# Kernel optimization log

Hardware: AMD Instinct MI355X
Metric: run time of the kernel (lower is better)

Reference implementation:

```python
import jax, jax.numpy as jnp
import numpy as np

NUM_NODES = 20000
EMB_DIM = 128
HIDDEN = 64
NUM_RELS = 8
NUM_CLASSES = 16
HEADS = 3
NUM_EDGES = 640000
NEG_SLOPE = 0.2


def setup_inputs() -> dict:
    key = jax.random.key(0)
    ks = jax.random.split(key, 12)
    edge_index = jax.random.randint(ks[0], (2, NUM_EDGES), 0, NUM_NODES, dtype=jnp.int32)
    edge_type = jax.random.randint(ks[1], (NUM_EDGES,), 0, NUM_RELS, dtype=jnp.int32)
    s1 = 1.0 / np.sqrt(EMB_DIM)
    s2 = 1.0 / np.sqrt(HIDDEN)
    return {
        "emb": jax.random.normal(ks[2], (NUM_NODES, EMB_DIM), jnp.float32),
        "w1": jax.random.normal(ks[3], (NUM_RELS, EMB_DIM, HEADS * HIDDEN), jnp.float32) * s1,
        "q1": jax.random.normal(ks[4], (HEADS * HIDDEN, HEADS), jnp.float32) * s2,
        "k1": jax.random.normal(ks[5], (HEADS * HIDDEN, HEADS), jnp.float32) * s2,
        "b1": jnp.zeros((HIDDEN,), jnp.float32),
        "w2": jax.random.normal(ks[6], (NUM_RELS, HIDDEN, HEADS * NUM_CLASSES), jnp.float32) * s2,
        "q2": jax.random.normal(ks[7], (HEADS * NUM_CLASSES, HEADS), jnp.float32) * 0.1,
        "k2": jax.random.normal(ks[8], (HEADS * NUM_CLASSES, HEADS), jnp.float32) * 0.1,
        "b2": jnp.zeros((NUM_CLASSES,), jnp.float32),
        "edge_index": edge_index,
        "edge_type": edge_type,
    }


def _rgat_conv(x, w, q, k, b, src, dst, edge_type, heads, out_ch):
    # Per-relation node transform [R, N, heads*out]; equivalent to x_e @ w[edge_type[e]]
    n = x.shape[0]
    xr = jnp.einsum('nd,rdo->rno', x, w)
    out_i = xr[edge_type, dst]  # [E, heads*out] (destination, x_i)
    out_j = xr[edge_type, src]  # [E, heads*out] (source, x_j)
    # additive self-attention with dim=1: alpha [E, heads]
    alpha = jax.nn.leaky_relu(out_i @ q + out_j @ k, negative_slope=NEG_SLOPE)
    # across-relation segment softmax over destination index (PyG utils.softmax)
    amax = jax.ops.segment_max(alpha, dst, num_segments=n)
    amax = jnp.where(jnp.isneginf(amax), 0.0, amax)
    ex = jnp.exp(alpha - amax[dst])
    denom = jax.ops.segment_sum(ex, dst, num_segments=n)
    alpha = ex / (denom[dst] + 1e-16)
    # weighted messages, scatter-add aggregation
    msg = alpha[:, :, None] * out_j.reshape(-1, heads, out_ch)  # [E, heads, out]
    aggr = jax.ops.segment_sum(msg, dst, num_segments=n)  # [N, heads, out]
    # concat=False -> mean over heads, then bias [out]
    return aggr.mean(axis=1) + b


def reference(emb, w1, q1, k1, b1, w2, q2, k2, b2, edge_index, edge_type):
    src, dst = edge_index[0], edge_index[1]
    x1 = _rgat_conv(emb, w1, q1, k1, b1, src, dst, edge_type, HEADS, HIDDEN)
    x2 = jax.nn.relu(x1)
    x3 = _rgat_conv(x2, w2, q2, k2, b2, src, dst, edge_type, HEADS, NUM_CLASSES)
    return jax.nn.sigmoid(x3)
```

## Files before the change

kernel.cpp:

```cpp
#include <hip/hip_runtime.h>
#include <hip/hip_bf16.h>
#include <math.h>

#define N_NODES 20000
#define EMB 128
#define HID 64
#define RELS 8
#define CLS 16
#define N_EDGES 640000
#define NEG 0.2f
#define NKEYS (N_NODES * RELS)
#define SCAN_CHUNK 1024
#define SCAN_NBLK ((NKEYS + SCAN_CHUNK - 1) / SCAN_CHUNK)

typedef unsigned short ushort_t;
typedef __attribute__((ext_vector_type(8))) short bf16x8;
typedef __attribute__((ext_vector_type(8))) unsigned short ushort8_t;
typedef __attribute__((ext_vector_type(4))) unsigned short ushort4_t;
typedef __attribute__((ext_vector_type(4))) float f32x4;

__device__ __forceinline__ float b2f(ushort_t u) {
    return __uint_as_float(((unsigned int)u) << 16);
}
__device__ __forceinline__ ushort_t f2b(float f) {
    __hip_bfloat16 h = __float2bfloat16(f);
    return *reinterpret_cast<ushort_t*>(&h);
}

__global__ __launch_bounds__(256) void k_cvt(const float* __restrict__ in, ushort_t* __restrict__ outp, int n4) {
    int i = blockIdx.x * blockDim.x + threadIdx.x;
    if (i >= n4) return;
    float4 v = *(const float4*)&in[(size_t)i * 4];
    ushort4 o;
    o.x = f2b(v.x); o.y = f2b(v.y); o.z = f2b(v.z); o.w = f2b(v.w);
    *(ushort4*)&outp[(size_t)i * 4] = o;
}

template <int D, int OUT>
__global__ __launch_bounds__(256) void k_wqk(const float* __restrict__ w, const float* __restrict__ q,
                                             const float* __restrict__ k, ushort_t* __restrict__ wqkt) {
    int tid = blockIdx.x * blockDim.x + threadIdx.x;
    if (tid >= 48 * D) return;
    int c = tid / D, i = tid % D;
    int r = c / 6, j = c % 6;
    const float* qk = (j < 3) ? q : k;
    int jj = (j < 3) ? j : j - 3;
    const float* wrow = w + ((size_t)r * D + i) * OUT;
    float s = 0.f;
    for (int o = 0; o < OUT; o++) s += wrow[o] * qk[o * 3 + jj];
    wqkt[(size_t)c * D + i] = f2b(s);
}

template <int D, int OC>
__global__ __launch_bounds__(256) void k_wagg(const float* __restrict__ w, ushort_t* __restrict__ outp) {
    const int KT = RELS * 3 * D;
    int tid = blockIdx.x * blockDim.x + threadIdx.x;
    if (tid >= OC * KT) return;
    int o = tid / KT, kidx = tid % KT;
    int r = kidx / (3 * D), h = (kidx / D) % 3, i = kidx % D;
    float v = w[((size_t)r * D + i) * (3 * OC) + h * OC + o];
    outp[tid] = f2b(v);
}

__global__ __launch_bounds__(256) void k_count(const int* __restrict__ dst, const int* __restrict__ et,
                                               int* __restrict__ counts) {
    int e = blockIdx.x * blockDim.x + threadIdx.x;
    if (e < N_EDGES) atomicAdd(&counts[dst[e] * 8 + et[e]], 1);
}

__global__ __launch_bounds__(256) void k_scanA(const int* __restrict__ counts, int* __restrict__ keyoff,
                                               int* __restrict__ blocksum) {
    __shared__ int part[256];
    int b = blockIdx.x, tid = threadIdx.x;
    int base = b * SCAN_CHUNK + tid * 4;
    int4 c = make_int4(0, 0, 0, 0);
    if (base + 3 < NKEYS) c = *(const int4*)&counts[base];
    else {
        if (base + 0 < NKEYS) c.x = counts[base + 0];
        if (base + 1 < NKEYS) c.y = counts[base + 1];
        if (base + 2 < NKEYS) c.z = counts[base + 2];
        if (base + 3 < NKEYS) c.w = counts[base + 3];
    }
    int s = c.x + c.y + c.z + c.w;
    part[tid] = s;
    __syncthreads();
    for (int off = 1; off < 256; off <<= 1) {
        int v = (tid >= off) ? part[tid - off] : 0;
        __syncthreads();
        part[tid] += v;
        __syncthreads();
    }
    int excl = part[tid] - s;
    int4 o;
    o.x = excl;
    o.y = excl + c.x;
    o.z = excl + c.x + c.y;
    o.w = excl + c.x + c.y + c.z;
    if (base + 3 < NKEYS) *(int4*)&keyoff[base] = o;
    else {
        if (base + 0 < NKEYS) keyoff[base + 0] = o.x;
        if (base + 1 < NKEYS) keyoff[base + 1] = o.y;
        if (base + 2 < NKEYS) keyoff[base + 2] = o.z;
        if (base + 3 < NKEYS) keyoff[base + 3] = o.w;
    }
    if (tid == 255) blocksum[b] = part[255];
}

__global__ __launch_bounds__(256) void k_scanB(int* __restrict__ blocksum, int* __restrict__ blockbase,
                                               int* __restrict__ keyoff) {
    __shared__ int part[256];
    int tid = threadIdx.x;
    int v0 = (tid < SCAN_NBLK) ? blocksum[tid] : 0;
    part[tid] = v0;
    __syncthreads();
    for (int off = 1; off < 256; off <<= 1) {
        int v = (tid >= off) ? part[tid - off] : 0;
        __syncthreads();
        part[tid] += v;
        __syncthreads();
    }
    if (tid < SCAN_NBLK) blockbase[tid] = part[tid] - v0;
    if (tid == 255) keyoff[NKEYS] = part[255];
}

__global__ __launch_bounds__(256) void k_scanC(const int* __restrict__ blockbase, int* __restrict__ keyoff,
                                               int* __restrict__ cursor) {
    int b = blockIdx.x, tid = threadIdx.x;
    int base = b * SCAN_CHUNK + tid * 4;
    int add = blockbase[b];
    if (base + 3 < NKEYS) {
        int4 v = *(const int4*)&keyoff[base];
        v.x += add; v.y += add; v.z += add; v.w += add;
        *(int4*)&keyoff[base] = v;
        *(int4*)&cursor[base] = v;
    } else {
        for (int j = 0; j < 4; j++) {
            if (base + j < NKEYS) {
                int v = keyoff[base + j] + add;
                keyoff[base + j] = v;
                cursor[base + j] = v;
            }
        }
    }
}

__global__ __launch_bounds__(256) void k_scatter(const int* __restrict__ src, const int* __restrict__ dst,
                                                 const int* __restrict__ et, int* __restrict__ cursor,
                                                 int* __restrict__ srcs) {
    int e = blockIdx.x * blockDim.x + threadIdx.x;
    if (e < N_EDGES) {
        int p = atomicAdd(&cursor[dst[e] * 8 + et[e]], 1);
        srcs[p] = src[e];
    }
}

template <int K, int KCH, int N, int MREP, int NREP>
__global__ __launch_bounds__(256) void k_mfma_gemm(const ushort_t* __restrict__ A, const ushort_t* __restrict__ Bt,
                                                   float* __restrict__ outp, int M) {
    const int wid = threadIdx.x >> 6;
    const int lane = threadIdx.x & 63;
    const int m0 = blockIdx.x * (4 * MREP * 16) + wid * (MREP * 16);
    const int kbase = blockIdx.y * KCH;
    const int l15 = lane & 15;
    const int kq = (lane >> 4) * 8;

    f32x4 acc[MREP][NREP] = {};
    for (int kk = kbase; kk < kbase + KCH; kk += 32) {
        bf16x8 a[MREP], b[NREP];
#pragma unroll
        for (int i = 0; i < MREP; i++) {
            int row = m0 + i * 16 + l15;
            row = row < M ? row : M - 1;
            a[i] = *(const bf16x8*)&A[(size_t)row * K + kk + kq];
        }
#pragma unroll
        for (int j = 0; j < NREP; j++) b[j] = *(const bf16x8*)&Bt[(size_t)(j * 16 + l15) * K + kk + kq];
#pragma unroll
        for (int i = 0; i < MREP; i++)
#pragma unroll
            for (int j = 0; j < NREP; j++)
                acc[i][j] = __builtin_amdgcn_mfma_f32_16x16x32_bf16(a[i], b[j], acc[i][j], 0, 0, 0);
    }
    float* op = outp + (size_t)blockIdx.y * M * N;
    const int r4 = (lane >> 4) * 4;
#pragma unroll
    for (int i = 0; i < MREP; i++) {
#pragma unroll
        for (int j = 0; j < NREP; j++) {
#pragma unroll
            for (int g = 0; g < 4; g++) {
                int row = m0 + i * 16 + r4 + g;
                if (row < M) op[(size_t)row * N + j * 16 + l15] = acc[i][j][g];
            }
        }
    }
}

__device__ __forceinline__ void edge_alpha(int s_idx, const int (&ko)[9], const int* __restrict__ srcs,
                                           const float* __restrict__ qkd, const float* __restrict__ qbase,
                                           float& a0, float& a1, float& a2, int& sv) {
    int r = 0;
#pragma unroll
    for (int j = 1; j < 8; j++) r += (s_idx >= ko[j]) ? 1 : 0;
    sv = srcs[s_idx];
    const float* kd = qkd + (size_t)sv * 48 + r * 6 + 3;
    const float* qd = qbase + r * 6;
    float t0 = qd[0] + kd[0], t1 = qd[1] + kd[1], t2 = qd[2] + kd[2];
    a0 = t0 > 0.f ? t0 : NEG * t0;
    a1 = t1 > 0.f ? t1 : NEG * t1;
    a2 = t2 > 0.f ? t2 : NEG * t2;
}

__global__ __launch_bounds__(256) void k_stats(const int* __restrict__ keyoff, const int* __restrict__ srcs,
                                               const float* __restrict__ qkd, float4* __restrict__ svw) {
    int node = blockIdx.x * 4 + (threadIdx.x >> 6);
    int lane = threadIdx.x & 63;
    int ko[9];
#pragma unroll
    for (int j = 0; j < 9; j++) ko[j] = keyoff[node * 8 + j];
    int beg = ko[0], end = ko[8], deg = end - beg;
    if (deg == 0) return;
    const float* qbase = qkd + (size_t)node * 48;

    if (deg <= 64) {
        float a0 = -INFINITY, a1 = -INFINITY, a2 = -INFINITY;
        int sv = 0;
        if (lane < deg) edge_alpha(beg + lane, ko, srcs, qkd, qbase, a0, a1, a2, sv);
        float m0 = a0, m1 = a1, m2 = a2;
#pragma unroll
        for (int off = 32; off >= 1; off >>= 1) {
            m0 = fmaxf(m0, __shfl_xor(m0, off));
            m1 = fmaxf(m1, __shfl_xor(m1, off));
            m2 = fmaxf(m2, __shfl_xor(m2, off));
        }
        float e0 = 0.f, e1 = 0.f, e2 = 0.f;
        if (lane < deg) {
            e0 = expf(a0 - m0);
            e1 = expf(a1 - m1);
            e2 = expf(a2 - m2);
        }
        float s0 = e0, s1 = e1, s2 = e2;
#pragma unroll
        for (int off = 32; off >= 1; off >>= 1) {
            s0 += __shfl_xor(s0, off);
            s1 += __shfl_xor(s1, off);
            s2 += __shfl_xor(s2, off);
        }
        float i0 = 1.f / (3.f * (s0 + 1e-16f));
        float i1 = 1.f / (3.f * (s1 + 1e-16f));
        float i2 = 1.f / (3.f * (s2 + 1e-16f));
        if (lane < deg)
            svw[beg + lane] = make_float4(__int_as_float(sv), e0 * i0, e1 * i1, e2 * i2);
    } else {
        float m0 = -INFINITY, m1 = -INFINITY, m2 = -INFINITY;
        for (int i = beg + lane; i < end; i += 64) {
            float a0, a1, a2; int sv;
            edge_alpha(i, ko, srcs, qkd, qbase, a0, a1, a2, sv);
            m0 = fmaxf(m0, a0); m1 = fmaxf(m1, a1); m2 = fmaxf(m2, a2);
        }
#pragma unroll
        for (int off = 32; off >= 1; off >>= 1) {
            m0 = fmaxf(m0, __shfl_xor(m0, off));
            m1 = fmaxf(m1, __shfl_xor(m1, off));
            m2 = fmaxf(m2, __shfl_xor(m2, off));
        }
        float s0 = 0.f, s1 = 0.f, s2 = 0.f;
        for (int i = beg + lane; i < end; i += 64) {
            float a0, a1, a2; int sv;
            edge_alpha(i, ko, srcs, qkd, qbase, a0, a1, a2, sv);
            s0 += expf(a0 - m0); s1 += expf(a1 - m1); s2 += expf(a2 - m2);
        }
#pragma unroll
        for (int off = 32; off >= 1; off >>= 1) {
            s0 += __shfl_xor(s0, off);
            s1 += __shfl_xor(s1, off);
            s2 += __shfl_xor(s2, off);
        }
        float i0 = 1.f / (3.f * (s0 + 1e-16f));
        float i1 = 1.f / (3.f * (s1 + 1e-16f));
        float i2 = 1.f / (3.f * (s2 + 1e-16f));
        for (int i = beg + lane; i < end; i += 64) {
            float a0, a1, a2; int sv;
            edge_alpha(i, ko, srcs, qkd, qbase, a0, a1, a2, sv);
            svw[i] = make_float4(__int_as_float(sv), expf(a0 - m0) * i0, expf(a1 - m1) * i1, expf(a2 - m2) * i2);
        }
    }
}

#define PADK1 408
__global__ __launch_bounds__(256) void k_fused1(const int* __restrict__ keyoff, const float4* __restrict__ svw,
                                                const ushort_t* __restrict__ x, const ushort_t* __restrict__ wagg,
                                                float* __restrict__ part) {
    __shared__ ushort_t lt[16][PADK1];
    const int tid = threadIdx.x;
    const int w = tid >> 6, lane = tid & 63;
    const int q15 = lane & 15, kq = (lane >> 4) * 8;
    const int l15 = lane & 15;
    const int nbase = blockIdx.x * 16;
    const int r = blockIdx.y;
    const int mynode = w * 4 + (lane >> 4);
    const int key = (nbase + mynode) * 8 + r;

    const int beg = keyoff[key], end = keyoff[key + 1];
    float a0[8] = {}, a1[8] = {}, a2[8] = {};
    for (int s = beg; s < end; s++) {
        float4 sw = svw[s];
        int sv = __float_as_int(sw.x);
        ushort8_t xv = *(const ushort8_t*)&x[(size_t)sv * 128 + q15 * 8];
#pragma unroll
        for (int c = 0; c < 8; c++) {
            float f = b2f(xv[c]);
            a0[c] += sw.y * f;
            a1[c] += sw.z * f;
            a2[c] += sw.w * f;
        }
    }
    ushort8_t o0, o1, o2;
#pragma unroll
    for (int c = 0; c < 8; c++) {
        o0[c] = f2b(a0[c]);
        o1[c] = f2b(a1[c]);
        o2[c] = f2b(a2[c]);
    }
    *(ushort8_t*)&lt[mynode][0 * 128 + q15 * 8] = o0;
    *(ushort8_t*)&lt[mynode][1 * 128 + q15 * 8] = o1;
    *(ushort8_t*)&lt[mynode][2 * 128 + q15 * 8] = o2;
    __syncthreads();

    f32x4 acc = {};
#pragma unroll
    for (int ks = 0; ks < 12; ks++) {
        bf16x8 av = *(const bf16x8*)&lt[l15][ks * 32 + kq];
        bf16x8 bv = *(const bf16x8*)&wagg[(size_t)(w * 16 + l15) * 3072 + r * 384 + ks * 32 + kq];
        acc = __builtin_amdgcn_mfma_f32_16x16x32_bf16(av, bv, acc, 0, 0, 0);
    }
    float* op = part + (size_t)r * N_NODES * 64;
    const int r4 = (lane >> 4) * 4;
#pragma unroll
    for (int g = 0; g < 4; g++) {
        int row = nbase + r4 + g;
        op[(size_t)row * 64 + w * 16 + l15] = acc[g];
    }
}

#define PADK2 208
__global__ __launch_bounds__(256) void k_fused2(const int* __restrict__ keyoff, const float4* __restrict__ svw,
                                                const ushort_t* __restrict__ x2in, const ushort_t* __restrict__ wagg,
                                                float* __restrict__ part) {
    __shared__ ushort_t lt[16][PADK2];
    const int tid = threadIdx.x;
    const int w = tid >> 6, lane = tid & 63;
    const int q15 = lane & 15, kq = (lane >> 4) * 8;
    const int l15 = lane & 15;
    const int nbase = blockIdx.x * 16;
    const int r = blockIdx.y;
    const int mynode = w * 4 + (lane >> 4);
    const int key = (nbase + mynode) * 8 + r;

    const int beg = keyoff[key], end = keyoff[key + 1];
    float a0[4] = {}, a1[4] = {}, a2[4] = {};
    for (int s = beg; s < end; s++) {
        float4 sw = svw[s];
        int sv = __float_as_int(sw.x);
        ushort4_t xv = *(const ushort4_t*)&x2in[(size_t)sv * 64 + q15 * 4];
#pragma unroll
        for (int c = 0; c < 4; c++) {
            float f = b2f(xv[c]);
            a0[c] += sw.y * f;
            a1[c] += sw.z * f;
            a2[c] += sw.w * f;
        }
    }
    ushort4_t o0, o1, o2;
#pragma unroll
    for (int c = 0; c < 4; c++) {
        o0[c] = f2b(a0[c]);
        o1[c] = f2b(a1[c]);
        o2[c] = f2b(a2[c]);
    }
    *(ushort4_t*)&lt[mynode][0 * 64 + q15 * 4] = o0;
    *(ushort4_t*)&lt[mynode][1 * 64 + q15 * 4] = o1;
    *(ushort4_t*)&lt[mynode][2 * 64 + q15 * 4] = o2;
    __syncthreads();

    if (w == 0) {
        f32x4 acc = {};
#pragma unroll
        for (int ks = 0; ks < 6; ks++) {
            bf16x8 av = *(const bf16x8*)&lt[l15][ks * 32 + kq];
            bf16x8 bv = *(const bf16x8*)&wagg[(size_t)l15 * 1536 + r * 192 + ks * 32 + kq];
            acc = __builtin_amdgcn_mfma_f32_16x16x32_bf16(av, bv, acc, 0, 0, 0);
        }
        const int r4 = (lane >> 4) * 4;
#pragma unroll
        for (int g = 0; g < 4; g++)
            part[(size_t)r * N_NODES * 16 + (size_t)(nbase + r4 + g) * 16 + l15] = acc[g];
    }
}

__global__ __launch_bounds__(256) void k_reduce1(const float* __restrict__ part, const float* __restrict__ bias,
                                                 ushort_t* __restrict__ x2) {
    int idx = blockIdx.x * blockDim.x + threadIdx.x;
    const int MN = N_NODES * 64;
    if (idx >= MN) return;
    float s = bias[idx & 63];
#pragma unroll
    for (int r = 0; r < 8; r++) s += part[idx + (size_t)r * MN];
    x2[idx] = f2b(s > 0.f ? s : 0.f);
}

__global__ __launch_bounds__(256) void k_reduce2(const float* __restrict__ part, const float* __restrict__ bias,
                                                 float* __restrict__ outp) {
    int idx = blockIdx.x * blockDim.x + threadIdx.x;
    const int MN = N_NODES * 16;
    if (idx >= MN) return;
    float s = bias[idx & 15];
#pragma unroll
    for (int r = 0; r < 8; r++) s += part[idx + (size_t)r * MN];
    outp[idx] = 1.f / (1.f + expf(-s));
}

extern "C" void kernel_launch(void* const* d_in, const int* in_sizes, int n_in, void* d_out, int out_size,
                              void* d_ws, size_t ws_size, hipStream_t stream) {
    const float* emb = (const float*)d_in[0];
    const float* w1 = (const float*)d_in[1];
    const float* q1 = (const float*)d_in[2];
    const float* k1 = (const float*)d_in[3];
    const float* b1 = (const float*)d_in[4];
    const float* w2 = (const float*)d_in[5];
    const float* q2 = (const float*)d_in[6];
    const float* k2 = (const float*)d_in[7];
    const float* b2 = (const float*)d_in[8];
    const int* eidx = (const int*)d_in[9];
    const int* etype = (const int*)d_in[10];
    const int* srcv = eidx;
    const int* dstv = eidx + N_EDGES;
    float* out = (float*)d_out;

    char* p = (char*)d_ws;
    auto alloc = [&](size_t bytes) -> void* {
        void* q = p;
        p += (bytes + 255) & ~(size_t)255;
        return q;
    };
    int* counts = (int*)alloc((size_t)NKEYS * 4);
    int* keyoff = (int*)alloc((size_t)(NKEYS + 1) * 4);
    int* cursor = (int*)alloc((size_t)NKEYS * 4);
    int* blocksum = (int*)alloc((size_t)SCAN_NBLK * 4);
    int* blockbase = (int*)alloc((size_t)SCAN_NBLK * 4);
    int* srcs = (int*)alloc((size_t)N_EDGES * 4);
    float4* svw = (float4*)alloc((size_t)N_EDGES * 16);
    ushort_t* emb_b = (ushort_t*)alloc((size_t)N_NODES * EMB * 2);
    ushort_t* wqkt1 = (ushort_t*)alloc((size_t)48 * 128 * 2);
    ushort_t* wagg1 = (ushort_t*)alloc((size_t)64 * 3072 * 2);
    ushort_t* wqkt2 = (ushort_t*)alloc((size_t)48 * 64 * 2);
    ushort_t* wagg2 = (ushort_t*)alloc((size_t)16 * 1536 * 2);
    float* qkd = (float*)alloc((size_t)N_NODES * 48 * 4);
    ushort_t* x2 = (ushort_t*)alloc((size_t)N_NODES * 64 * 2);
    float* partials = (float*)alloc((size_t)8 * N_NODES * 64 * 4);

    k_cvt<<<(N_NODES * EMB / 4 + 255) / 256, 256, 0, stream>>>(emb, emb_b, N_NODES * EMB / 4);
    k_wqk<128, 192><<<(48 * 128 + 255) / 256, 256, 0, stream>>>(w1, q1, k1, wqkt1);
    k_wqk<64, 48><<<(48 * 64 + 255) / 256, 256, 0, stream>>>(w2, q2, k2, wqkt2);
    k_wagg<128, 64><<<(64 * 3072 + 255) / 256, 256, 0, stream>>>(w1, wagg1);
    k_wagg<64, 16><<<(16 * 1536 + 255) / 256, 256, 0, stream>>>(w2, wagg2);

    hipMemsetAsync(counts, 0, (size_t)NKEYS * 4, stream);
    k_count<<<(N_EDGES + 255) / 256, 256, 0, stream>>>(dstv, etype, counts);
    k_scanA<<<SCAN_NBLK, 256, 0, stream>>>(counts, keyoff, blocksum);
    k_scanB<<<1, 256, 0, stream>>>(blocksum, blockbase, keyoff);
    k_scanC<<<SCAN_NBLK, 256, 0, stream>>>(blockbase, keyoff, cursor);
    k_scatter<<<(N_EDGES + 255) / 256, 256, 0, stream>>>(srcv, dstv, etype, cursor, srcs);

    k_mfma_gemm<128, 128, 48, 1, 3><<<dim3(313, 1), 256, 0, stream>>>(emb_b, wqkt1, qkd, N_NODES);
    k_stats<<<N_NODES / 4, 256, 0, stream>>>(keyoff, srcs, qkd, svw);
    k_fused1<<<dim3(N_NODES / 16, 8), 256, 0, stream>>>(keyoff, svw, emb_b, wagg1, partials);
    k_reduce1<<<(N_NODES * 64 + 255) / 256, 256, 0, stream>>>(partials, b1, x2);

    k_mfma_gemm<64, 64, 48, 1, 3><<<dim3(313, 1), 256, 0, stream>>>(x2, wqkt2, qkd, N_NODES);
    k_stats<<<N_NODES / 4, 256, 0, stream>>>(keyoff, srcs, qkd, svw);
    k_fused2<<<dim3(N_NODES / 16, 8), 256, 0, stream>>>(keyoff, svw, x2, wagg2, partials);
    k_reduce2<<<(N_NODES * 16 + 255) / 256, 256, 0, stream>>>(partials, b2, out);
}
```

Before: 262.4 us.

## Merge weight/embedding prep kernels into one launch and software-pipeline gather loops

Result: faster. 243.8 us (-7.1%).

```diff
diff --git a/kernel.cpp b/kernel.cpp
--- a/kernel.cpp
+++ b/kernel.cpp
@@ -27,9 +27,7 @@
     return *reinterpret_cast<ushort_t*>(&h);
 }
 
-__global__ __launch_bounds__(256) void k_cvt(const float* __restrict__ in, ushort_t* __restrict__ outp, int n4) {
-    int i = blockIdx.x * blockDim.x + threadIdx.x;
-    if (i >= n4) return;
+__device__ __forceinline__ void prep_cvt(int i, const float* __restrict__ in, ushort_t* __restrict__ outp) {
     float4 v = *(const float4*)&in[(size_t)i * 4];
     ushort4 o;
     o.x = f2b(v.x); o.y = f2b(v.y); o.z = f2b(v.z); o.w = f2b(v.w);
@@ -37,10 +35,8 @@
 }
 
 template <int D, int OUT>
-__global__ __launch_bounds__(256) void k_wqk(const float* __restrict__ w, const float* __restrict__ q,
-                                             const float* __restrict__ k, ushort_t* __restrict__ wqkt) {
-    int tid = blockIdx.x * blockDim.x + threadIdx.x;
-    if (tid >= 48 * D) return;
+__device__ __forceinline__ void prep_wqk(int tid, const float* __restrict__ w, const float* __restrict__ q,
+                                         const float* __restrict__ k, ushort_t* __restrict__ wqkt) {
     int c = tid / D, i = tid % D;
     int r = c / 6, j = c % 6;
     const float* qk = (j < 3) ? q : k;
@@ -52,14 +48,37 @@
 }
 
 template <int D, int OC>
-__global__ __launch_bounds__(256) void k_wagg(const float* __restrict__ w, ushort_t* __restrict__ outp) {
+__device__ __forceinline__ void prep_wagg(int tid, const float* __restrict__ w, ushort_t* __restrict__ outp) {
     const int KT = RELS * 3 * D;
-    int tid = blockIdx.x * blockDim.x + threadIdx.x;
-    if (tid >= OC * KT) return;
-    int o = tid / KT, kidx = tid % KT;
+    int kidx = tid % KT;
+    int o = tid / KT;
     int r = kidx / (3 * D), h = (kidx / D) % 3, i = kidx % D;
-    float v = w[((size_t)r * D + i) * (3 * OC) + h * OC + o];
-    outp[tid] = f2b(v);
+    outp[tid] = f2b(w[((size_t)r * D + i) * (3 * OC) + h * OC + o]);
+}
+
+#define PREP_N0 (N_NODES * EMB / 4)
+#define PREP_N1 (48 * 128)
+#define PREP_N2 (48 * 64)
+#define PREP_N3 (64 * 3072)
+#define PREP_N4 (16 * 1536)
+#define PREP_TOT (PREP_N0 + PREP_N1 + PREP_N2 + PREP_N3 + PREP_N4)
+
+__global__ __launch_bounds__(256) void k_prep(const float* __restrict__ emb, ushort_t* __restrict__ emb_b,
+                                              const float* __restrict__ w1, const float* __restrict__ q1,
+                                              const float* __restrict__ k1, ushort_t* __restrict__ wqkt1,
+                                              const float* __restrict__ w2, const float* __restrict__ q2,
+                                              const float* __restrict__ k2, ushort_t* __restrict__ wqkt2,
+                                              ushort_t* __restrict__ wagg1, ushort_t* __restrict__ wagg2) {
+    int tid = blockIdx.x * 256 + threadIdx.x;
+    if (tid < PREP_N0) { prep_cvt(tid, emb, emb_b); return; }
+    tid -= PREP_N0;
+    if (tid < PREP_N1) { prep_wqk<128, 192>(tid, w1, q1, k1, wqkt1); return; }
+    tid -= PREP_N1;
+    if (tid < PREP_N2) { prep_wqk<64, 48>(tid, w2, q2, k2, wqkt2); return; }
+    tid -= PREP_N2;
+    if (tid < PREP_N3) { prep_wagg<128, 64>(tid, w1, wagg1); return; }
+    tid -= PREP_N3;
+    if (tid < PREP_N4) { prep_wagg<64, 16>(tid, w2, wagg2); return; }
 }
 
 __global__ __launch_bounds__(256) void k_count(const int* __restrict__ dst, const int* __restrict__ et,
@@ -302,17 +321,35 @@
     const int key = (nbase + mynode) * 8 + r;
 
     const int beg = keyoff[key], end = keyoff[key + 1];
+    const int deg = end - beg;
     float a0[8] = {}, a1[8] = {}, a2[8] = {};
-    for (int s = beg; s < end; s++) {
-        float4 sw = svw[s];
-        int sv = __float_as_int(sw.x);
-        ushort8_t xv = *(const ushort8_t*)&x[(size_t)sv * 128 + q15 * 8];
-#pragma unroll
-        for (int c = 0; c < 8; c++) {
-            float f = b2f(xv[c]);
-            a0[c] += sw.y * f;
-            a1[c] += sw.z * f;
-            a2[c] += sw.w * f;
+    if (deg > 0) {
+        float4 sw0 = svw[beg];
+        float4 sw1;
+        {
+            int s = beg + 1;
+            sw1 = svw[s < end ? s : beg];
+            if (1 >= deg) { sw1.y = 0.f; sw1.z = 0.f; sw1.w = 0.f; }
+        }
+        ushort8_t xv0 = *(const ushort8_t*)&x[(size_t)__float_as_int(sw0.x) * 128 + q15 * 8];
+        for (int i = 0; i < deg; i++) {
+            float4 sw2;
+            {
+                int s = beg + i + 2;
+                sw2 = svw[s < end ? s : beg];
+                if (i + 2 >= deg) { sw2.y = 0.f; sw2.z = 0.f; sw2.w = 0.f; }
+            }
+            ushort8_t xv1 = *(const ushort8_t*)&x[(size_t)__float_as_int(sw1.x) * 128 + q15 * 8];
+#pragma unroll
+            for (int c = 0; c < 8; c++) {
+                float f = b2f(xv0[c]);
+                a0[c] += sw0.y * f;
+                a1[c] += sw0.z * f;
+                a2[c] += sw0.w * f;
+            }
+            sw0 = sw1;
+            sw1 = sw2;
+            xv0 = xv1;
         }
     }
     ushort8_t o0, o1, o2;
@@ -358,17 +395,35 @@
     const int key = (nbase + mynode) * 8 + r;
 
     const int beg = keyoff[key], end = keyoff[key + 1];
+    const int deg = end - beg;
     float a0[4] = {}, a1[4] = {}, a2[4] = {};
-    for (int s = beg; s < end; s++) {
-        float4 sw = svw[s];
-        int sv = __float_as_int(sw.x);
-        ushort4_t xv = *(const ushort4_t*)&x2in[(size_t)sv * 64 + q15 * 4];
-#pragma unroll
-        for (int c = 0; c < 4; c++) {
-            float f = b2f(xv[c]);
-            a0[c] += sw.y * f;
-            a1[c] += sw.z * f;
-            a2[c] += sw.w * f;
+    if (deg > 0) {
+        float4 sw0 = svw[beg];
+        float4 sw1;
+        {
+            int s = beg + 1;
+            sw1 = svw[s < end ? s : beg];
+            if (1 >= deg) { sw1.y = 0.f; sw1.z = 0.f; sw1.w = 0.f; }
+        }
+        ushort4_t xv0 = *(const ushort4_t*)&x2in[(size_t)__float_as_int(sw0.x) * 64 + q15 * 4];
+        for (int i = 0; i < deg; i++) {
+            float4 sw2;
+            {
+                int s = beg + i + 2;
+                sw2 = svw[s < end ? s : beg];
+                if (i + 2 >= deg) { sw2.y = 0.f; sw2.z = 0.f; sw2.w = 0.f; }
+            }
+            ushort4_t xv1 = *(const ushort4_t*)&x2in[(size_t)__float_as_int(sw1.x) * 64 + q15 * 4];
+#pragma unroll
+            for (int c = 0; c < 4; c++) {
+                float f = b2f(xv0[c]);
+                a0[c] += sw0.y * f;
+                a1[c] += sw0.z * f;
+                a2[c] += sw0.w * f;
+            }
+            sw0 = sw1;
+            sw1 = sw2;
+            xv0 = xv1;
         }
     }
     ushort4_t o0, o1, o2;
@@ -459,11 +514,8 @@
     ushort_t* x2 = (ushort_t*)alloc((size_t)N_NODES * 64 * 2);
     float* partials = (float*)alloc((size_t)8 * N_NODES * 64 * 4);
 
-    k_cvt<<<(N_NODES * EMB / 4 + 255) / 256, 256, 0, stream>>>(emb, emb_b, N_NODES * EMB / 4);
-    k_wqk<128, 192><<<(48 * 128 + 255) / 256, 256, 0, stream>>>(w1, q1, k1, wqkt1);
-    k_wqk<64, 48><<<(48 * 64 + 255) / 256, 256, 0, stream>>>(w2, q2, k2, wqkt2);
-    k_wagg<128, 64><<<(64 * 3072 + 255) / 256, 256, 0, stream>>>(w1, wagg1);
-    k_wagg<64, 16><<<(16 * 1536 + 255) / 256, 256, 0, stream>>>(w2, wagg2);
+    k_prep<<<(PREP_TOT + 255) / 256, 256, 0, stream>>>(emb, emb_b, w1, q1, k1, wqkt1, w2, q2, k2, wqkt2, wagg1,
+                                                       wagg2);
 
     hipMemsetAsync(counts, 0, (size_t)NKEYS * 4, stream);
     k_count<<<(N_EDGES + 255) / 256, 256, 0, stream>>>(dstv, etype, counts);
```
